# Performance work log

Hardware: AMD Instinct MI355X
Metric: run time of the kernel (lower is better)

Reference implementation:

```python
import jax, jax.numpy as jnp
import numpy as np

B, T, C, H = 2, 2048, 1024, 16
HD = C // H          # head dim = 64
HD2 = HD // 2        # rotary half = 32


def setup_inputs() -> dict:
    key = jax.random.key(0)
    k0, k1, k2 = jax.random.split(key, 3)
    x = jax.random.normal(k0, (B, T, C), jnp.float32)
    Wqkv = jax.random.normal(k1, (C, 3 * C), jnp.float32) * (1.0 / np.sqrt(C))
    bqkv = jnp.zeros((3 * C,), jnp.float32)
    Wproj = jax.random.normal(k2, (C, C), jnp.float32) * (1.0 / np.sqrt(C))
    bproj = jnp.zeros((C,), jnp.float32)
    # standard rotary frequencies: theta_i = 10000^{-2i/hd}
    inv_freq = 1.0 / (10000.0 ** (jnp.arange(0, HD, 2, dtype=jnp.float32) / HD))
    angles = jnp.arange(T, dtype=jnp.float32)[:, None] * inv_freq[None, :]  # (T, HD2)
    return {
        "x": x,
        "freqs_cos": jnp.cos(angles),
        "freqs_sin": jnp.sin(angles),
        "Wqkv": Wqkv,
        "bqkv": bqkv,
        "Wproj": Wproj,
        "bproj": bproj,
    }


def _rope(u, cos, sin):
    # u: (B, T, H, HD); half-split pairing: (u[i], u[i + HD/2]) form a complex pair
    u1, u2 = u[..., :HD2], u[..., HD2:]
    c = cos[None, :, None, :]  # (1, T, 1, HD2)
    s = sin[None, :, None, :]
    return jnp.concatenate([u1 * c - u2 * s, u1 * s + u2 * c], axis=-1)


def reference(x, freqs_cos, freqs_sin, Wqkv, bqkv, Wproj, bproj):
    Bc, Tc, Cc = x.shape
    qkv = x @ Wqkv + bqkv                      # (B, T, 3C)
    q, k, v = jnp.split(qkv, 3, axis=-1)
    q = q.reshape(Bc, Tc, H, HD)
    k = k.reshape(Bc, Tc, H, HD)
    v = v.reshape(Bc, Tc, H, HD)
    q = _rope(q, freqs_cos, freqs_sin)
    k = _rope(k, freqs_cos, freqs_sin)
    scale = 1.0 / np.sqrt(HD)
    scores = jnp.einsum("bthd,bshd->bhts", q, k) * scale  # (B, H, T, T)
    causal = jnp.tril(jnp.ones((Tc, Tc), dtype=bool))
    scores = jnp.where(causal[None, None], scores, jnp.finfo(scores.dtype).min)
    p = jax.nn.softmax(scores, axis=-1)
    y = jnp.einsum("bhts,bshd->bthd", p, v).reshape(Bc, Tc, Cc)
    return y @ Wproj + bproj
```

## Files before the change

### kernel.cpp

```cpp
#include <hip/hip_runtime.h>
#include <hip/hip_bf16.h>
#include <cstdint>
#include <cmath>

typedef __bf16 bf16_t;
typedef __attribute__((ext_vector_type(8))) __bf16 bf16x8;
typedef __attribute__((ext_vector_type(4))) float f32x4;

#define LOG2E 1.4426950408889634f

constexpr int B_ = 2, T_ = 2048, C_ = 1024, H_ = 16, HD_ = 64, HD2_ = 32;
constexpr int M_ = B_ * T_;

static __device__ __forceinline__ f32x4 mfma16(bf16x8 a, bf16x8 b, f32x4 c) {
    return __builtin_amdgcn_mfma_f32_16x16x32_bf16(a, b, c, 0, 0, 0);
}

#define GLL(gp, lp)                                                          \
    __builtin_amdgcn_global_load_lds(                                        \
        (const __attribute__((address_space(1))) void*)(gp),                 \
        (__attribute__((address_space(3))) void*)(lp), 16, 0, 0)

__global__ void prep(const float* __restrict__ x, bf16_t* __restrict__ xb,
                     const float* __restrict__ Wqkv, bf16_t* __restrict__ wqkvT,
                     const float* __restrict__ Wproj, bf16_t* __restrict__ wprojT) {
    __shared__ float tile[32][33];
    const int bid = blockIdx.x, tid = threadIdx.x;
    if (bid < 4096) {
        int i = bid * 256 + tid;
        float4 v = ((const float4*)x)[i];
        bf16_t o[4] = {(bf16_t)v.x, (bf16_t)v.y, (bf16_t)v.z, (bf16_t)v.w};
        *(uint64_t*)(xb + (size_t)i * 4) = *(uint64_t*)o;
        return;
    }
    const float* W;
    bf16_t* WT;
    int K, N, nb, kb;
    if (bid < 4096 + 3072) {
        int t = bid - 4096;
        W = Wqkv; WT = wqkvT; K = C_; N = 3 * C_;
        nb = (t % 96) * 32; kb = (t / 96) * 32;
    } else {
        int t = bid - 7168;
        W = Wproj; WT = wprojT; K = C_; N = C_;
        nb = (t & 31) * 32; kb = (t >> 5) * 32;
    }
    int tx = tid & 31, ty = tid >> 5;
    for (int i = ty; i < 32; i += 8)
        tile[i][tx] = W[(size_t)(kb + i) * N + nb + tx];
    __syncthreads();
    for (int i = ty; i < 32; i += 8)
        WT[(size_t)(nb + i) * K + kb + tx] = (bf16_t)tile[tx][i];
}

template <int MODE>
__global__ __launch_bounds__(256, 3) void gemm128(
    const bf16_t* __restrict__ A, const bf16_t* __restrict__ BT, const float* __restrict__ bias,
    int N, int K,
    bf16_t* __restrict__ Qb, bf16_t* __restrict__ Kb, bf16_t* __restrict__ VTb,
    const float* __restrict__ cosT, const float* __restrict__ sinT, float* __restrict__ out) {
    __shared__ alignas(16) bf16_t As[128 * 32];
    __shared__ alignas(16) bf16_t Bs[128 * 32];
    const int tid = threadIdx.x;
    const int w = tid >> 6, lane = tid & 63;
    const int quad = lane >> 4, r = lane & 15;
    const int wm = (w >> 1) * 64, wn = (w & 1) * 64;
    const int bid = blockIdx.x;
    const int xcd = bid & 7, s = bid >> 3;
    const int nbs = N >> 8;
    const int mb = ((((xcd >> 1) << 3) + (s & 7))) << 7;
    const int nb = (((xcd & 1) * nbs + (s >> 3))) << 7;
    const int row_st = tid >> 2, seg = tid & 3;

    f32x4 acc[4][4] = {};

    const bf16_t* gA0 = A + (size_t)(mb + row_st) * K + seg * 8;
    const bf16_t* gA1 = A + (size_t)(mb + row_st + 64) * K + seg * 8;
    const bf16_t* gB0 = BT + (size_t)(nb + row_st) * K + seg * 8;
    const bf16_t* gB1 = BT + (size_t)(nb + row_st + 64) * K + seg * 8;

    for (int k0 = 0; k0 < K; k0 += 32) {
        __syncthreads();
        GLL(gA0 + k0, As + tid * 8);
        GLL(gA1 + k0, As + 2048 + tid * 8);
        GLL(gB0 + k0, Bs + tid * 8);
        GLL(gB1 + k0, Bs + 2048 + tid * 8);
        __syncthreads();
        bf16x8 af[4], bfr[4];
#pragma unroll
        for (int i = 0; i < 4; i++) af[i] = *(const bf16x8*)(As + (wm + i * 16 + r) * 32 + quad * 8);
#pragma unroll
        for (int j = 0; j < 4; j++) bfr[j] = *(const bf16x8*)(Bs + (wn + j * 16 + r) * 32 + quad * 8);
#pragma unroll
        for (int i = 0; i < 4; i++)
#pragma unroll
            for (int j = 0; j < 4; j++) acc[i][j] = mfma16(af[i], bfr[j], acc[i][j]);
    }

    if (MODE == 0) {
        const int col_base = nb + wn;
        const int region = col_base >> 10;
        const int h = (col_base & 1023) >> 6;
        const float qscale = 0.125f * LOG2E;
        if (region < 2) {
#pragma unroll
            for (int i = 0; i < 4; i++) {
#pragma unroll
                for (int g = 0; g < 4; g++) {
                    int m = mb + wm + i * 16 + quad * 4 + g;
                    int b = m >> 11, t = m & (T_ - 1);
                    bf16_t* dst = (region == 0 ? Qb : Kb) + ((size_t)((b * H_ + h) * T_ + t)) * 64;
                    int tw = t & 7;
#pragma unroll
                    for (int j = 0; j < 2; j++) {
                        int d = j * 16 + r;
                        float u1 = acc[i][j][g] + bias[col_base + d];
                        float u2 = acc[i][j + 2][g] + bias[col_base + d + 32];
                        float c = cosT[t * HD2_ + d], s2 = sinT[t * HD2_ + d];
                        float o1 = u1 * c - u2 * s2;
                        float o2 = u1 * s2 + u2 * c;
                        if (region == 0) {
                            dst[d] = (bf16_t)(o1 * qscale);
                            dst[d + 32] = (bf16_t)(o2 * qscale);
                        } else {
                            dst[((((d >> 3) ^ tw)) << 3) | (d & 7)] = (bf16_t)o1;
                            dst[(((((d + 32) >> 3) ^ tw)) << 3) | (d & 7)] = (bf16_t)o2;
                        }
                    }
                }
            }
        } else {
#pragma unroll
            for (int i = 0; i < 4; i++) {
                int m0 = mb + wm + i * 16 + quad * 4;
                int b = m0 >> 11, t0 = m0 & (T_ - 1);
                bf16_t* base = VTb + (size_t)(b * H_ + h) * 64 * T_;
#pragma unroll
                for (int j = 0; j < 4; j++) {
                    int d = j * 16 + r;
                    float bb = bias[col_base + d];
                    bf16_t pk[4];
#pragma unroll
                    for (int g = 0; g < 4; g++) pk[g] = (bf16_t)(acc[i][j][g] + bb);
                    int c = (((t0 >> 3) & 7) ^ (d & 7));
                    int tsw = (t0 & ~63) | (c << 3) | (t0 & 7);
                    *(uint64_t*)(base + (size_t)d * T_ + tsw) = *(uint64_t*)pk;
                }
            }
        }
    } else {
#pragma unroll
        for (int i = 0; i < 4; i++)
#pragma unroll
            for (int g = 0; g < 4; g++) {
                int m = mb + wm + i * 16 + quad * 4 + g;
#pragma unroll
                for (int j = 0; j < 4; j++) {
                    int col = nb + wn + j * 16 + r;
                    out[(size_t)m * N + col] = acc[i][j][g] + bias[col];
                }
            }
    }
}

__global__ __launch_bounds__(512, 4) void attn64(
    const bf16_t* __restrict__ Qb, const bf16_t* __restrict__ Kb,
    const bf16_t* __restrict__ VTb, bf16_t* __restrict__ att) {
    __shared__ alignas(16) bf16_t Ks[2][2][4096];
    __shared__ alignas(16) bf16_t Vs[2][2][4096];
    __shared__ alignas(16) bf16_t Ps[8][1024];
    const int tid = threadIdx.x;
    const int w = tid >> 6, lane = tid & 63;
    const int grp = w >> 2, wq = w & 3;
    const int quad = lane >> 4, r = lane & 15;
    const int id = blockIdx.x;
    const int t = 31 - (id >> 5);
    const int bh = id & 31;
    const int ntiles = t + 1, nstages = (t + 2) >> 1;
    const size_t kbase = (size_t)bh * T_ * 64;
    const size_t vbase = (size_t)bh * 64 * T_;
    bf16_t* Pw = &Ps[w][0];
    const int srow = tid >> 3, schunk = tid & 7;
    const int koff0 = ((quad ^ (r & 7)) * 8);
    const int koff1 = (((quad + 4) ^ (r & 7)) * 8);

    const int qrow = t * 64 + wq * 16 + r;
    bf16x8 qf0 = *(const bf16x8*)(Qb + kbase + (size_t)qrow * 64 + quad * 8);
    bf16x8 qf1 = *(const bf16x8*)(Qb + kbase + (size_t)qrow * 64 + 32 + quad * 8);

    f32x4 oacc[4] = {};
    float l = 0.f;

    {
        const bf16_t* kg = Kb + kbase + (size_t)srow * 64 + schunk * 8;
        GLL(kg, &Ks[0][0][0] + tid * 8);
        const bf16_t* vg = VTb + vbase + (size_t)srow * T_ + schunk * 8;
        GLL(vg, &Vs[0][0][0] + tid * 8);
        if (1 < ntiles) {
            GLL(kg + 64 * 64, &Ks[0][1][0] + tid * 8);
            GLL(vg + 64, &Vs[0][1][0] + tid * 8);
        }
    }
    for (int s = 0; s < nstages; s++) {
        const int cur = s & 1;
        __syncthreads();
        if (s + 1 < nstages) {
            const int ja = 2 * (s + 1);
            const bf16_t* kg = Kb + kbase + (size_t)(ja * 64 + srow) * 64 + schunk * 8;
            const bf16_t* vg = VTb + vbase + (size_t)srow * T_ + ja * 64 + schunk * 8;
            GLL(kg, &Ks[cur ^ 1][0][0] + tid * 8);
            GLL(vg, &Vs[cur ^ 1][0][0] + tid * 8);
            if (ja + 1 < ntiles) {
                GLL(kg + 64 * 64, &Ks[cur ^ 1][1][0] + tid * 8);
                GLL(vg + 64, &Vs[cur ^ 1][1][0] + tid * 8);
            }
        }
        const int jt = 2 * s + grp;
        if (jt < ntiles) {
            const bf16_t* Kt = &Ks[cur][grp][0];
            const bf16_t* Vt = &Vs[cur][grp][0];
            f32x4 sc[4];
#pragma unroll
            for (int m0 = 0; m0 < 4; m0++) {
                const bf16_t* kp = Kt + (m0 * 16 + r) * 64;
                bf16x8 kf0 = *(const bf16x8*)(kp + koff0);
                bf16x8 kf1 = *(const bf16x8*)(kp + koff1);
                f32x4 z = {0.f, 0.f, 0.f, 0.f};
                z = mfma16(kf0, qf0, z);
                z = mfma16(kf1, qf1, z);
                sc[m0] = z;
            }
            if (jt == t) {
                const int j0 = jt * 64;
#pragma unroll
                for (int m0 = 0; m0 < 4; m0++) {
                    int kvb = j0 + m0 * 16 + quad * 4;
#pragma unroll
                    for (int g = 0; g < 4; g++)
                        if (kvb + g > qrow) sc[m0][g] = -INFINITY;
                }
            }
            float rs = 0.f;
#pragma unroll
            for (int m0 = 0; m0 < 4; m0++)
#pragma unroll
                for (int g = 0; g < 4; g++) {
                    float pp = __builtin_amdgcn_exp2f(sc[m0][g]);
                    sc[m0][g] = pp;
                    rs += pp;
                }
            l += rs;
#pragma unroll
            for (int m0 = 0; m0 < 4; m0++) {
                bf16_t hq[4];
#pragma unroll
                for (int g = 0; g < 4; g++) hq[g] = (bf16_t)sc[m0][g];
                int elem = (m0 >> 1) * 512 + (((m0 & 1) * 2 + (quad >> 1)) * 16 + r) * 8 + (quad & 1) * 4;
                *(uint64_t*)(Pw + elem) = *(uint64_t*)hq;
            }
            __builtin_amdgcn_wave_barrier();
            bf16x8 pf0 = *(const bf16x8*)(Pw + lane * 8);
            bf16x8 pf1 = *(const bf16x8*)(Pw + 512 + lane * 8);
#pragma unroll
            for (int d0 = 0; d0 < 4; d0++) {
                const bf16_t* vp = Vt + (d0 * 16 + r) * 64;
                bf16x8 vf0 = *(const bf16x8*)(vp + koff0);
                bf16x8 vf1 = *(const bf16x8*)(vp + koff1);
                oacc[d0] = mfma16(vf0, pf0, oacc[d0]);
                oacc[d0] = mfma16(vf1, pf1, oacc[d0]);
            }
            __builtin_amdgcn_wave_barrier();
        }
    }
    l += __shfl_xor(l, 16);
    l += __shfl_xor(l, 32);
    __syncthreads();
    float* Co = (float*)&Ks[0][0][0];
    float* Cl = (float*)&Vs[0][0][0];
    if (grp == 1) {
#pragma unroll
        for (int d0 = 0; d0 < 4; d0++)
            *(f32x4*)(Co + wq * 1024 + r * 64 + d0 * 16 + quad * 4) = oacc[d0];
        if (quad == 0) Cl[wq * 16 + r] = l;
    }
    __syncthreads();
    if (grp == 0) {
        float inv = 1.f / (l + Cl[wq * 16 + r]);
        const int b = bh >> 4, h = bh & 15;
        bf16_t* dst = att + ((size_t)(b * T_ + qrow)) * 1024 + h * 64;
#pragma unroll
        for (int d0 = 0; d0 < 4; d0++) {
            f32x4 o1 = *(const f32x4*)(Co + wq * 1024 + r * 64 + d0 * 16 + quad * 4);
            bf16_t hh[4];
#pragma unroll
            for (int g = 0; g < 4; g++)
                hh[g] = (bf16_t)((oacc[d0][g] + o1[g]) * inv);
            *(uint64_t*)(dst + d0 * 16 + quad * 4) = *(uint64_t*)hh;
        }
    }
}

extern "C" void kernel_launch(void* const* d_in, const int* in_sizes, int n_in,
                              void* d_out, int out_size, void* d_ws, size_t ws_size,
                              hipStream_t stream) {
    const float* x = (const float*)d_in[0];
    const float* fcos = (const float*)d_in[1];
    const float* fsin = (const float*)d_in[2];
    const float* Wqkv = (const float*)d_in[3];
    const float* bqkv = (const float*)d_in[4];
    const float* Wproj = (const float*)d_in[5];
    const float* bproj = (const float*)d_in[6];
    float* out = (float*)d_out;

    uint8_t* p = (uint8_t*)d_ws;
    size_t need = 0;
    auto take = [&](size_t bytes) {
        void* q = p;
        size_t pad = (bytes + 255) & ~(size_t)255;
        p += pad;
        need += pad;
        return q;
    };
    bf16_t* xb = (bf16_t*)take((size_t)M_ * C_ * 2);
    bf16_t* wqkvT = (bf16_t*)take((size_t)3 * C_ * C_ * 2);
    bf16_t* wprojT = (bf16_t*)take((size_t)C_ * C_ * 2);
    bf16_t* Qb = (bf16_t*)take((size_t)B_ * H_ * T_ * 64 * 2);
    bf16_t* Kb = (bf16_t*)take((size_t)B_ * H_ * T_ * 64 * 2);
    bf16_t* VTb = (bf16_t*)take((size_t)B_ * H_ * 64 * T_ * 2);
    bf16_t* attb = (bf16_t*)take((size_t)M_ * C_ * 2);
    if (ws_size < need) return;

    prep<<<8192, 256, 0, stream>>>(x, xb, Wqkv, wqkvT, Wproj, wprojT);

    gemm128<0><<<dim3(768), 256, 0, stream>>>(
        xb, wqkvT, bqkv, 3 * C_, C_, Qb, Kb, VTb, fcos, fsin, nullptr);

    attn64<<<dim3(1024), 512, 0, stream>>>(Qb, Kb, VTb, attb);

    gemm128<1><<<dim3(256), 256, 0, stream>>>(
        attb, wprojT, bproj, C_, C_, nullptr, nullptr, nullptr, nullptr, nullptr, out);
}
```

Measured before the change: 186.0 us.

## Swizzle GEMM LDS tiles and halve proj GEMM N-tile to fill more CUs

Applies an XOR swizzle to the 16-byte segment position in the LDS tiles of both GEMMs. The global load address and the fragment read offset are permuted consistently, which is meant to reduce LDS bank conflicts on the fragment reads. For the output projection GEMM, the N tile shrinks from 128 to 64 and the grid doubles to 512 blocks, so more of the CUs have work in that small GEMM. The trade-off is lower operand reuse per block and more A-tile reloads.

Measured after the change: 179.2 us. -3.7%, faster.

```diff
diff --git a/kernel.cpp b/kernel.cpp
--- a/kernel.cpp
+++ b/kernel.cpp
@@ -59,42 +59,50 @@
     int N, int K,
     bf16_t* __restrict__ Qb, bf16_t* __restrict__ Kb, bf16_t* __restrict__ VTb,
     const float* __restrict__ cosT, const float* __restrict__ sinT, float* __restrict__ out) {
+    constexpr int NT = (MODE == 1) ? 2 : 4;
     __shared__ alignas(16) bf16_t As[128 * 32];
-    __shared__ alignas(16) bf16_t Bs[128 * 32];
+    __shared__ alignas(16) bf16_t Bs[32 * NT * 32];
     const int tid = threadIdx.x;
     const int w = tid >> 6, lane = tid & 63;
     const int quad = lane >> 4, r = lane & 15;
-    const int wm = (w >> 1) * 64, wn = (w & 1) * 64;
+    const int wm = (w >> 1) * 64, wn = (w & 1) * (16 * NT);
     const int bid = blockIdx.x;
     const int xcd = bid & 7, s = bid >> 3;
-    const int nbs = N >> 8;
-    const int mb = ((((xcd >> 1) << 3) + (s & 7))) << 7;
-    const int nb = (((xcd & 1) * nbs + (s >> 3))) << 7;
+    int mb, nb;
+    if (MODE == 0) {
+        mb = (((xcd >> 1) << 3) + (s & 7)) << 7;
+        nb = (((xcd & 1) * 12 + (s >> 3))) << 7;
+    } else {
+        mb = (((xcd >> 1) << 3) + (s & 7)) << 7;
+        nb = (((xcd & 1) << 3) + (s >> 3)) << 6;
+    }
     const int row_st = tid >> 2, seg = tid & 3;
-
-    f32x4 acc[4][4] = {};
-
-    const bf16_t* gA0 = A + (size_t)(mb + row_st) * K + seg * 8;
-    const bf16_t* gA1 = A + (size_t)(mb + row_st + 64) * K + seg * 8;
-    const bf16_t* gB0 = BT + (size_t)(nb + row_st) * K + seg * 8;
-    const bf16_t* gB1 = BT + (size_t)(nb + row_st + 64) * K + seg * 8;
+    const int sw = (row_st >> 1) & 3;
+    const int aoff = (quad ^ ((r >> 1) & 3)) * 8;
+
+    f32x4 acc[4][NT] = {};
+
+    const bf16_t* gA0 = A + (size_t)(mb + row_st) * K + (seg ^ sw) * 8;
+    const bf16_t* gA1 = A + (size_t)(mb + row_st + 64) * K + (seg ^ sw) * 8;
+    const bf16_t* gB0 = BT + (size_t)(nb + row_st) * K + (seg ^ sw) * 8;
+    const bf16_t* gB1 = (NT == 4) ? BT + (size_t)(nb + row_st + 64) * K + (seg ^ sw) * 8 : nullptr;
 
     for (int k0 = 0; k0 < K; k0 += 32) {
         __syncthreads();
         GLL(gA0 + k0, As + tid * 8);
         GLL(gA1 + k0, As + 2048 + tid * 8);
         GLL(gB0 + k0, Bs + tid * 8);
-        GLL(gB1 + k0, Bs + 2048 + tid * 8);
+        if (NT == 4) GLL(gB1 + k0, Bs + 2048 + tid * 8);
         __syncthreads();
-        bf16x8 af[4], bfr[4];
-#pragma unroll
-        for (int i = 0; i < 4; i++) af[i] = *(const bf16x8*)(As + (wm + i * 16 + r) * 32 + quad * 8);
-#pragma unroll
-        for (int j = 0; j < 4; j++) bfr[j] = *(const bf16x8*)(Bs + (wn + j * 16 + r) * 32 + quad * 8);
+        bf16x8 af[4], bfr[NT];
+#pragma unroll
+        for (int i = 0; i < 4; i++) af[i] = *(const bf16x8*)(As + (wm + i * 16 + r) * 32 + aoff);
+#pragma unroll
+        for (int j = 0; j < NT; j++) bfr[j] = *(const bf16x8*)(Bs + (wn + j * 16 + r) * 32 + aoff);
 #pragma unroll
         for (int i = 0; i < 4; i++)
 #pragma unroll
-            for (int j = 0; j < 4; j++) acc[i][j] = mfma16(af[i], bfr[j], acc[i][j]);
+            for (int j = 0; j < NT; j++) acc[i][j] = mfma16(af[i], bfr[j], acc[i][j]);
     }
 
     if (MODE == 0) {
@@ -155,7 +163,7 @@
             for (int g = 0; g < 4; g++) {
                 int m = mb + wm + i * 16 + quad * 4 + g;
 #pragma unroll
-                for (int j = 0; j < 4; j++) {
+                for (int j = 0; j < NT; j++) {
                     int col = nb + wn + j * 16 + r;
                     out[(size_t)m * N + col] = acc[i][j][g] + bias[col];
                 }
@@ -337,6 +345,6 @@
 
     attn64<<<dim3(1024), 512, 0, stream>>>(Qb, Kb, VTb, attb);
 
-    gemm128<1><<<dim3(256), 256, 0, stream>>>(
+    gemm128<1><<<dim3(512), 256, 0, stream>>>(
         attb, wprojT, bproj, C_, C_, nullptr, nullptr, nullptr, nullptr, nullptr, out);
 }
```
